# Kernel optimization log

Measured on AMD Instinct MI355X. Metric: run time of the kernel, lower is better.

The kernel has to match this reference:

```python
import jax, jax.numpy as jnp
import numpy as np

N = 100000
E = 1600000
D_IN = 256
D_OUT = 128
ALPHA = 0.2  # LeakyReLU negative slope


def setup_inputs() -> dict:
    key = jax.random.key(0)
    k1, k2, k3, k4, k5 = jax.random.split(key, 5)
    x = jax.random.normal(k1, (N, D_IN), dtype=jnp.float32)
    # random edges + self-loops so every destination row has >=1 incoming edge
    src = jax.random.randint(k2, (E - N,), 0, N)
    dst = jax.random.randint(k3, (E - N,), 0, N)
    loops = jnp.arange(N)
    edge = jnp.stack([jnp.concatenate([src, loops]),
                      jnp.concatenate([dst, loops])]).astype(jnp.int64)  # [2, E]
    W = jax.random.normal(k4, (D_IN, D_OUT), dtype=jnp.float32) * 0.1
    a = jax.random.normal(k5, (1, 2 * D_OUT), dtype=jnp.float32) * 0.1
    return {"x": x, "edge": edge, "W": W, "a": a}


def reference(x, edge, W, a):
    n = x.shape[0]
    d_out = W.shape[1]
    h = x @ W  # [n, d_out]
    src, dst = edge[0], edge[1]
    # a @ concat(h[src], h[dst]) decomposes into two per-node projections
    f_src = h @ a[0, :d_out]   # [n]
    f_dst = h @ a[0, d_out:]   # [n]
    tmp = f_src[src] + f_dst[dst]                      # [E]
    lrelu = jnp.where(tmp > 0, tmp, ALPHA * tmp)
    edge_e = jnp.exp(-lrelu)                           # [E]
    # spmm(A, ones) -> rowsum; spmm(A, h) -> weighted aggregation (rows = src)
    e_rowsum = jax.ops.segment_sum(edge_e, src, num_segments=n)           # [n]
    hh = jax.ops.segment_sum(edge_e[:, None] * h[dst], src, num_segments=n)  # [n, d_out]
    hh = hh / e_rowsum[:, None]
    return jax.nn.elu(hh)  # end=False -> apply ELU
```

## Files before the change

kernel.cpp:

```cpp
#include <hip/hip_runtime.h>

#define D_IN 256
#define D_OUT 128
#define ALPHA 0.2f
#define RB 64
#define RBSH 6
#define NBMAX 1600
#define CH 8192
#define CAPG 1536
#define OVFCAP 32768
#define LKH 128

typedef __attribute__((ext_vector_type(8))) short bf16x8;
typedef __attribute__((ext_vector_type(4))) float f32x4;

__device__ inline unsigned short f2bf(float f) {
    unsigned int u = __float_as_uint(f);
    return (unsigned short)((u + 0x7FFFu + ((u >> 16) & 1u)) >> 16);
}
__device__ inline float bf2f(unsigned short u) {
    return __uint_as_float(((unsigned int)u) << 16);
}
__device__ inline unsigned int cvt_pk_bf16(float lo, float hi) {
    unsigned int r;
    asm("v_cvt_pk_bf16_f32 %0, %1, %2" : "=v"(r) : "v"(lo), "v"(hi));
    return r;
}

__global__ __launch_bounds__(256) void k_wt(const float* __restrict__ W,
                                            unsigned short* __restrict__ WTb) {
    const int ncol = blockIdx.x;
    const int k = threadIdx.x;
    WTb[(size_t)ncol * 256 + k] = f2bf(W[(size_t)k * 128 + ncol]);
}

__global__ __launch_bounds__(256) void k_fused(const float* __restrict__ x,
                                               const unsigned short* __restrict__ WTb,
                                               const float* __restrict__ a,
                                               unsigned short* __restrict__ hb,
                                               float* __restrict__ f_src,
                                               float* __restrict__ f_dst, int n,
                                               const int* __restrict__ src,
                                               const int* __restrict__ dst,
                                               int* __restrict__ gcnt,
                                               int2* __restrict__ ovf,
                                               int* __restrict__ gkeys, int E, int nb,
                                               int nbf) {
    __shared__ char smem[128 * LKH * 2];
    __shared__ float sFp[128][2][2];
    const int t = threadIdx.x;

    if (blockIdx.x < nbf) {
        int* cnt = (int*)smem;
        int* bas = cnt + NBMAX;
        const int e0 = blockIdx.x * CH;
        const int e1 = min(e0 + CH, E);
        for (int i = t; i < nb; i += 256) cnt[i] = 0;
        __syncthreads();
        for (int e = e0 + t; e < e1; e += 256) atomicAdd(&cnt[src[e] >> RBSH], 1);
        __syncthreads();
        for (int b = t; b < nb; b += 256) {
            int c = cnt[b];
            bas[b] = c ? atomicAdd(&gcnt[b], c) : 0;
            cnt[b] = 0;
        }
        __syncthreads();
        for (int e = e0 + t; e < e1; e += 256) {
            int s = src[e], d = dst[e];
            int b = s >> RBSH;
            int key = ((s & (RB - 1)) << 17) | d;
            int r = bas[b] + atomicAdd(&cnt[b], 1);
            if (r < CAPG) {
                gkeys[b * CAPG + r] = key;
            } else {
                int o = atomicAdd(&gcnt[nb], 1);
                if (o < OVFCAP) ovf[o] = make_int2(b, key);
            }
        }
        return;
    }

    unsigned short* sA = (unsigned short*)smem;
    const int l = t & 63;
    const int w = t >> 6;
    const int wr = w >> 1, wc = w & 1;
    const int row0 = (blockIdx.x - nbf) * 128;
    const int col0 = wc * 64;
    const int lr = l & 15;
    const int g = l >> 4;
    const int lk8 = g * 8;

    f32x4 acc[4][4] = {};
    const unsigned short* bp[4];
    #pragma unroll
    for (int ni = 0; ni < 4; ++ni)
        bp[ni] = WTb + (size_t)(col0 + ni * 16 + lr) * 256 + lk8;

    #pragma unroll
    for (int half = 0; half < 2; ++half) {
        {
            const int rr = t >> 4;
            const int cc = (t & 15) * 8;
            #pragma unroll
            for (int it = 0; it < 8; ++it) {
                int r = it * 16 + rr;
                int gr = row0 + r;
                float4 fa, fb;
                if (gr < n) {
                    const float* xp = &x[(size_t)gr * D_IN + half * LKH + cc];
                    fa = *(const float4*)xp;
                    fb = *(const float4*)(xp + 4);
                } else {
                    fa = make_float4(0.f, 0.f, 0.f, 0.f);
                    fb = fa;
                }
                uint4 v;
                v.x = cvt_pk_bf16(fa.x, fa.y);
                v.y = cvt_pk_bf16(fa.z, fa.w);
                v.z = cvt_pk_bf16(fb.x, fb.y);
                v.w = cvt_pk_bf16(fb.z, fb.w);
                int js = (cc >> 3) ^ ((r & 7) << 1);
                *(uint4*)&sA[r * LKH + js * 8] = v;
            }
        }
        __syncthreads();

        #pragma unroll
        for (int k0 = 0; k0 < LKH; k0 += 32) {
            bf16x8 af[4], bfr[4];
            #pragma unroll
            for (int mi = 0; mi < 4; ++mi) {
                int row_l = wr * 64 + mi * 16 + lr;
                int js = ((k0 >> 3) + g) ^ ((row_l & 7) << 1);
                af[mi] = *(const bf16x8*)&sA[row_l * LKH + js * 8];
            }
            #pragma unroll
            for (int ni = 0; ni < 4; ++ni)
                bfr[ni] = *(const bf16x8*)(bp[ni] + half * LKH + k0);
            #pragma unroll
            for (int mi = 0; mi < 4; ++mi)
                #pragma unroll
                for (int ni = 0; ni < 4; ++ni)
                    acc[mi][ni] = __builtin_amdgcn_mfma_f32_16x16x32_bf16(
                        af[mi], bfr[ni], acc[mi][ni], 0, 0, 0);
        }
        __syncthreads();
    }

    #pragma unroll
    for (int mi = 0; mi < 4; ++mi) {
        #pragma unroll
        for (int q = 0; q < 4; ++q) {
            int r = wr * 64 + mi * 16 + g * 4 + q;
            unsigned int a01 = cvt_pk_bf16(acc[mi][0][q], acc[mi][1][q]);
            unsigned int a23 = cvt_pk_bf16(acc[mi][2][q], acc[mi][3][q]);
            int c0 = col0 + lr;
            int c1 = col0 + 16 + lr;
            int c2 = col0 + 32 + lr;
            int c3 = col0 + 48 + lr;
            int rx = (r & 7);
            sA[r * 128 + (((c0 >> 3) ^ rx) << 3) + (c0 & 7)] = (unsigned short)(a01 & 0xFFFF);
            sA[r * 128 + (((c1 >> 3) ^ rx) << 3) + (c1 & 7)] = (unsigned short)(a01 >> 16);
            sA[r * 128 + (((c2 >> 3) ^ rx) << 3) + (c2 & 7)] = (unsigned short)(a23 & 0xFFFF);
            sA[r * 128 + (((c3 >> 3) ^ rx) << 3) + (c3 & 7)] = (unsigned short)(a23 >> 16);
        }
    }
    __syncthreads();
    {
        const int rr2 = t >> 4;
        const int g82 = t & 15;
        #pragma unroll
        for (int it = 0; it < 8; ++it) {
            int r = it * 16 + rr2;
            int gs = g82 ^ (r & 7);
            bf16x8 v = *(const bf16x8*)&sA[r * 128 + gs * 8];
            int gr = row0 + r;
            if (gr < n)
                *(bf16x8*)&hb[(size_t)gr * D_OUT + g82 * 8] = v;
        }
    }

    float asv[4], adv[4];
    #pragma unroll
    for (int ni = 0; ni < 4; ++ni) {
        asv[ni] = a[col0 + ni * 16 + lr];
        adv[ni] = a[D_OUT + col0 + ni * 16 + lr];
    }
    #pragma unroll
    for (int mi = 0; mi < 4; ++mi) {
        #pragma unroll
        for (int q = 0; q < 4; ++q) {
            float fs = 0.f, fd = 0.f;
            #pragma unroll
            for (int ni = 0; ni < 4; ++ni) {
                float v = acc[mi][ni][q];
                fs = fmaf(v, asv[ni], fs);
                fd = fmaf(v, adv[ni], fd);
            }
            #pragma unroll
            for (int m = 1; m < 16; m <<= 1) {
                fs += __shfl_xor(fs, m);
                fd += __shfl_xor(fd, m);
            }
            if (lr == 0) {
                int rl = wr * 64 + mi * 16 + g * 4 + q;
                sFp[rl][wc][0] = fs;
                sFp[rl][wc][1] = fd;
            }
        }
    }
    __syncthreads();
    if (t < 128) {
        int r = row0 + t;
        if (r < n) {
            f_src[r] = sFp[t][0][0] + sFp[t][1][0];
            f_dst[r] = sFp[t][0][1] + sFp[t][1][1];
        }
    }
}

__global__ __launch_bounds__(512, 8) void k_bagg(const unsigned short* __restrict__ hb,
                                                 const float* __restrict__ f_src,
                                                 const float* __restrict__ f_dst,
                                                 const int* __restrict__ gcnt,
                                                 const int2* __restrict__ ovf,
                                                 const int* __restrict__ gkeys,
                                                 float* __restrict__ out, int n, int nb) {
    __shared__ int2 sdw[CAPG];
    __shared__ int nbase[RB];
    __shared__ int ncnt[RB];
    __shared__ int ncur[RB];
    __shared__ float fsl[RB];
    __shared__ int sc[RB];
    const int t = threadIdx.x;
    const int b = blockIdx.x;
    const int s0 = b * RB;
    const int nn = min(RB, n - s0);
    const int beg = b * CAPG;
    const int stored = min(gcnt[b], CAPG);
    const int ovf_n = min(gcnt[nb], OVFCAP);

    for (int i = t; i < RB; i += 512) {
        ncnt[i] = 0;
        fsl[i] = (i < nn) ? f_src[s0 + i] : 0.f;
    }
    __syncthreads();

    for (int i = t; i < stored; i += 512)
        atomicAdd(&ncnt[gkeys[beg + i] >> 17], 1);
    __syncthreads();

    if (t < RB) sc[t] = ncnt[t];
    __syncthreads();
    for (int off = 1; off < RB; off <<= 1) {
        int v = 0;
        if (t < RB && t >= off) v = sc[t - off];
        __syncthreads();
        if (t < RB) sc[t] += v;
        __syncthreads();
    }
    if (t < RB) {
        nbase[t] = sc[t] - ncnt[t];
        ncur[t]  = sc[t] - ncnt[t];
    }
    __syncthreads();

    for (int i = t; i < stored; i += 512) {
        int k = gkeys[beg + i];
        int d = k & 0x1FFFF, ls = k >> 17;
        float tmp = fsl[ls] + f_dst[d];
        float w = __expf(-((tmp > 0.f) ? tmp : ALPHA * tmp));
        int pos = atomicAdd(&ncur[ls], 1);
        sdw[pos] = make_int2(d, __float_as_int(w));
    }
    __syncthreads();

    const int lane = t & 63, wid = t >> 6;
    const int cl = (lane & 31) * 4;
    const bool isB = lane >= 32;
    for (int ni = wid; ni < nn; ni += 8) {
        const int jb = nbase[ni];
        const int cn = ncnt[ni];
        const int halfA = (cn + 1) >> 1;
        const int halfB = cn - halfA;
        const int lim = isB ? halfB : halfA;
        const int jbh = jb + (isB ? halfA : 0);
        float a0 = 0.f, a1 = 0.f, a2 = 0.f, a3 = 0.f, rowsum = 0.f;
        #pragma unroll 4
        for (int it = 0; it < halfA; ++it) {
            bool valid = it < lim;
            int2 dw = sdw[valid ? (jbh + it) : jb];
            float w = valid ? __int_as_float(dw.y) : 0.f;
            ushort4 hv = *(const ushort4*)&hb[(size_t)dw.x * D_OUT + cl];
            rowsum += w;
            a0 = fmaf(w, bf2f(hv.x), a0);
            a1 = fmaf(w, bf2f(hv.y), a1);
            a2 = fmaf(w, bf2f(hv.z), a2);
            a3 = fmaf(w, bf2f(hv.w), a3);
        }
        if (ovf_n > 0) {
            for (int o = 0; o < ovf_n; ++o) {
                int2 ov = ovf[o];
                if (ov.x == b && (ov.y >> 17) == ni && !isB) {
                    int d = ov.y & 0x1FFFF;
                    float tmp = fsl[ni] + f_dst[d];
                    float w = __expf(-((tmp > 0.f) ? tmp : ALPHA * tmp));
                    ushort4 hv = *(const ushort4*)&hb[(size_t)d * D_OUT + cl];
                    rowsum += w;
                    a0 = fmaf(w, bf2f(hv.x), a0);
                    a1 = fmaf(w, bf2f(hv.y), a1);
                    a2 = fmaf(w, bf2f(hv.z), a2);
                    a3 = fmaf(w, bf2f(hv.w), a3);
                }
            }
        }
        rowsum += __shfl_xor(rowsum, 32);
        a0 += __shfl_xor(a0, 32);
        a1 += __shfl_xor(a1, 32);
        a2 += __shfl_xor(a2, 32);
        a3 += __shfl_xor(a3, 32);
        if (!isB) {
            float inv = 1.f / rowsum;
            a0 *= inv; a1 *= inv; a2 *= inv; a3 *= inv;
            a0 = (a0 > 0.f) ? a0 : (__expf(a0) - 1.f);
            a1 = (a1 > 0.f) ? a1 : (__expf(a1) - 1.f);
            a2 = (a2 > 0.f) ? a2 : (__expf(a2) - 1.f);
            a3 = (a3 > 0.f) ? a3 : (__expf(a3) - 1.f);
            *(float4*)&out[(size_t)(s0 + ni) * D_OUT + cl] =
                make_float4(a0, a1, a2, a3);
        }
    }
}

extern "C" void kernel_launch(void* const* d_in, const int* in_sizes, int n_in,
                              void* d_out, int out_size, void* d_ws, size_t ws_size,
                              hipStream_t stream) {
    const float* x    = (const float*)d_in[0];
    const int*   edge = (const int*)d_in[1];
    const float* W    = (const float*)d_in[2];
    const float* a    = (const float*)d_in[3];
    float* out = (float*)d_out;

    const int n = in_sizes[0] / D_IN;
    const int E = in_sizes[1] / 2;
    const int* src = edge;
    const int* dst = edge + E;
    const int nb = (n + RB - 1) / RB;

    char* p = (char*)d_ws;
    unsigned short* hb  = (unsigned short*)p; p += (size_t)n * D_OUT * sizeof(unsigned short);
    unsigned short* WTb = (unsigned short*)p; p += (size_t)D_OUT * D_IN * sizeof(unsigned short);
    float* f_src = (float*)p;  p += (size_t)n * sizeof(float);
    float* f_dst = (float*)p;  p += (size_t)n * sizeof(float);
    int*  gcnt   = (int*)p;    p += (size_t)(nb + 1) * sizeof(int);
    int2* ovf    = (int2*)p;   p += (size_t)OVFCAP * sizeof(int2);
    int*  gkeys  = (int*)p;    p += (size_t)nb * CAPG * sizeof(int);

    const int gemm_blocks = (n + 127) / 128;
    const int nbf = (E + CH - 1) / CH;

    hipMemsetAsync(gcnt, 0, (size_t)(nb + 1) * sizeof(int), stream);
    k_wt<<<D_OUT, 256, 0, stream>>>(W, WTb);
    k_fused<<<nbf + gemm_blocks, 256, 0, stream>>>(x, WTb, a, hb, f_src, f_dst, n,
                                                   src, dst, gcnt, ovf, gkeys, E, nb, nbf);
    k_bagg<<<nb, 512, 0, stream>>>(hb, f_src, f_dst, gcnt, ovf, gkeys, out, n, nb);
}
```

Before: 134.8 us.

## Give each wave private 32-row GEMM tile to drop block barriers

The projection GEMM is restructured so each wave owns 32 full rows across all 128 output columns and stages its own x slice in a private LDS region, which removes every __syncthreads from the GEMM path. Because each wave covers all columns, the attention projections f_src/f_dst are finished in-wave and written directly, with no cross-wave LDS reduction. The h output is now written with scattered 2-byte global stores instead of going through LDS for coalesced 16-byte stores. In exchange, each wave loads twice as many W fragments per k-step, and the output writes are less coalesced.

```diff
diff --git a/kernel.cpp b/kernel.cpp
--- a/kernel.cpp
+++ b/kernel.cpp
@@ -9,7 +9,6 @@
 #define CH 8192
 #define CAPG 1536
 #define OVFCAP 32768
-#define LKH 128
 
 typedef __attribute__((ext_vector_type(8))) short bf16x8;
 typedef __attribute__((ext_vector_type(4))) float f32x4;
@@ -46,8 +45,7 @@
                                                int2* __restrict__ ovf,
                                                int* __restrict__ gkeys, int E, int nb,
                                                int nbf) {
-    __shared__ char smem[128 * LKH * 2];
-    __shared__ float sFp[128][2][2];
+    __shared__ char smem[32768];
     const int t = threadIdx.x;
 
     if (blockIdx.x < nbf) {
@@ -80,119 +78,94 @@
         return;
     }
 
-    unsigned short* sA = (unsigned short*)smem;
     const int l = t & 63;
     const int w = t >> 6;
-    const int wr = w >> 1, wc = w & 1;
-    const int row0 = (blockIdx.x - nbf) * 128;
-    const int col0 = wc * 64;
     const int lr = l & 15;
     const int g = l >> 4;
     const int lk8 = g * 8;
-
-    f32x4 acc[4][4] = {};
-    const unsigned short* bp[4];
+    const int row0 = (blockIdx.x - nbf) * 128 + w * 32;
+    unsigned short* sW = (unsigned short*)smem + w * 32 * 128;
+
+    f32x4 acc[2][8] = {};
+    const unsigned short* bp[8];
     #pragma unroll
-    for (int ni = 0; ni < 4; ++ni)
-        bp[ni] = WTb + (size_t)(col0 + ni * 16 + lr) * 256 + lk8;
-
-    #pragma unroll
+    for (int ni = 0; ni < 8; ++ni)
+        bp[ni] = WTb + (size_t)(ni * 16 + lr) * 256 + lk8;
+
     for (int half = 0; half < 2; ++half) {
-        {
-            const int rr = t >> 4;
-            const int cc = (t & 15) * 8;
-            #pragma unroll
-            for (int it = 0; it < 8; ++it) {
-                int r = it * 16 + rr;
-                int gr = row0 + r;
-                float4 fa, fb;
-                if (gr < n) {
-                    const float* xp = &x[(size_t)gr * D_IN + half * LKH + cc];
-                    fa = *(const float4*)xp;
-                    fb = *(const float4*)(xp + 4);
-                } else {
-                    fa = make_float4(0.f, 0.f, 0.f, 0.f);
-                    fb = fa;
-                }
-                uint4 v;
-                v.x = cvt_pk_bf16(fa.x, fa.y);
-                v.y = cvt_pk_bf16(fa.z, fa.w);
-                v.z = cvt_pk_bf16(fb.x, fb.y);
-                v.w = cvt_pk_bf16(fb.z, fb.w);
-                int js = (cc >> 3) ^ ((r & 7) << 1);
-                *(uint4*)&sA[r * LKH + js * 8] = v;
-            }
-        }
-        __syncthreads();
-
         #pragma unroll
-        for (int k0 = 0; k0 < LKH; k0 += 32) {
-            bf16x8 af[4], bfr[4];
-            #pragma unroll
-            for (int mi = 0; mi < 4; ++mi) {
-                int row_l = wr * 64 + mi * 16 + lr;
+        for (int it = 0; it < 8; ++it) {
+            int r = it * 4 + g;
+            int gr = row0 + r;
+            float4 fa, fb;
+            if (gr < n) {
+                const float* xp = &x[(size_t)gr * D_IN + half * 128 + lr * 8];
+                fa = *(const float4*)xp;
+                fb = *(const float4*)(xp + 4);
+            } else {
+                fa = make_float4(0.f, 0.f, 0.f, 0.f);
+                fb = fa;
+            }
+            uint4 v;
+            v.x = cvt_pk_bf16(fa.x, fa.y);
+            v.y = cvt_pk_bf16(fa.z, fa.w);
+            v.z = cvt_pk_bf16(fb.x, fb.y);
+            v.w = cvt_pk_bf16(fb.z, fb.w);
+            int js = lr ^ ((r & 7) << 1);
+            *(uint4*)&sW[r * 128 + js * 8] = v;
+        }
+
+        #pragma unroll
+        for (int k0 = 0; k0 < 128; k0 += 32) {
+            bf16x8 af[2], bfr[8];
+            #pragma unroll
+            for (int mi = 0; mi < 2; ++mi) {
+                int row_l = mi * 16 + lr;
                 int js = ((k0 >> 3) + g) ^ ((row_l & 7) << 1);
-                af[mi] = *(const bf16x8*)&sA[row_l * LKH + js * 8];
-            }
-            #pragma unroll
-            for (int ni = 0; ni < 4; ++ni)
-                bfr[ni] = *(const bf16x8*)(bp[ni] + half * LKH + k0);
-            #pragma unroll
-            for (int mi = 0; mi < 4; ++mi)
+                af[mi] = *(const bf16x8*)&sW[row_l * 128 + js * 8];
+            }
+            #pragma unroll
+            for (int ni = 0; ni < 8; ++ni)
+                bfr[ni] = *(const bf16x8*)(bp[ni] + half * 128 + k0);
+            #pragma unroll
+            for (int mi = 0; mi < 2; ++mi)
                 #pragma unroll
-                for (int ni = 0; ni < 4; ++ni)
+                for (int ni = 0; ni < 8; ++ni)
                     acc[mi][ni] = __builtin_amdgcn_mfma_f32_16x16x32_bf16(
                         af[mi], bfr[ni], acc[mi][ni], 0, 0, 0);
         }
-        __syncthreads();
     }
 
     #pragma unroll
-    for (int mi = 0; mi < 4; ++mi) {
+    for (int mi = 0; mi < 2; ++mi) {
         #pragma unroll
         for (int q = 0; q < 4; ++q) {
-            int r = wr * 64 + mi * 16 + g * 4 + q;
-            unsigned int a01 = cvt_pk_bf16(acc[mi][0][q], acc[mi][1][q]);
-            unsigned int a23 = cvt_pk_bf16(acc[mi][2][q], acc[mi][3][q]);
-            int c0 = col0 + lr;
-            int c1 = col0 + 16 + lr;
-            int c2 = col0 + 32 + lr;
-            int c3 = col0 + 48 + lr;
-            int rx = (r & 7);
-            sA[r * 128 + (((c0 >> 3) ^ rx) << 3) + (c0 & 7)] = (unsigned short)(a01 & 0xFFFF);
-            sA[r * 128 + (((c1 >> 3) ^ rx) << 3) + (c1 & 7)] = (unsigned short)(a01 >> 16);
-            sA[r * 128 + (((c2 >> 3) ^ rx) << 3) + (c2 & 7)] = (unsigned short)(a23 & 0xFFFF);
-            sA[r * 128 + (((c3 >> 3) ^ rx) << 3) + (c3 & 7)] = (unsigned short)(a23 >> 16);
-        }
-    }
-    __syncthreads();
-    {
-        const int rr2 = t >> 4;
-        const int g82 = t & 15;
-        #pragma unroll
-        for (int it = 0; it < 8; ++it) {
-            int r = it * 16 + rr2;
-            int gs = g82 ^ (r & 7);
-            bf16x8 v = *(const bf16x8*)&sA[r * 128 + gs * 8];
-            int gr = row0 + r;
-            if (gr < n)
-                *(bf16x8*)&hb[(size_t)gr * D_OUT + g82 * 8] = v;
-        }
-    }
-
-    float asv[4], adv[4];
+            int r = row0 + mi * 16 + g * 4 + q;
+            if (r < n) {
+                unsigned short* hp = &hb[(size_t)r * D_OUT + lr];
+                #pragma unroll
+                for (int np = 0; np < 4; ++np) {
+                    unsigned int pk = cvt_pk_bf16(acc[mi][2 * np][q], acc[mi][2 * np + 1][q]);
+                    hp[np * 32]      = (unsigned short)(pk & 0xFFFF);
+                    hp[np * 32 + 16] = (unsigned short)(pk >> 16);
+                }
+            }
+        }
+    }
+
+    float asv[8], adv[8];
     #pragma unroll
-    for (int ni = 0; ni < 4; ++ni) {
-        asv[ni] = a[col0 + ni * 16 + lr];
-        adv[ni] = a[D_OUT + col0 + ni * 16 + lr];
+    for (int ni = 0; ni < 8; ++ni) {
+        asv[ni] = a[ni * 16 + lr];
+        adv[ni] = a[D_OUT + ni * 16 + lr];
     }
     #pragma unroll
-    for (int mi = 0; mi < 4; ++mi) {
+    for (int mi = 0; mi < 2; ++mi) {
         #pragma unroll
         for (int q = 0; q < 4; ++q) {
             float fs = 0.f, fd = 0.f;
             #pragma unroll
-            for (int ni = 0; ni < 4; ++ni) {
+            for (int ni = 0; ni < 8; ++ni) {
                 float v = acc[mi][ni][q];
                 fs = fmaf(v, asv[ni], fs);
                 fd = fmaf(v, adv[ni], fd);
@@ -203,18 +176,12 @@
                 fd += __shfl_xor(fd, m);
             }
             if (lr == 0) {
-                int rl = wr * 64 + mi * 16 + g * 4 + q;
-                sFp[rl][wc][0] = fs;
-                sFp[rl][wc][1] = fd;
-            }
-        }
-    }
-    __syncthreads();
-    if (t < 128) {
-        int r = row0 + t;
-        if (r < n) {
-            f_src[r] = sFp[t][0][0] + sFp[t][1][0];
-            f_dst[r] = sFp[t][0][1] + sFp[t][1][1];
+                int r = row0 + mi * 16 + g * 4 + q;
+                if (r < n) {
+                    f_src[r] = fs;
+                    f_dst[r] = fd;
+                }
+            }
         }
     }
 }
```

Result: slower. 145.4 us (+7.8%).
